# Kernel tuning notes

Hardware: AMD Instinct MI355X
Metric: run time of the kernel (lower is better)

Reference implementation:

```python
import jax, jax.numpy as jnp
import numpy as np

N = 50000   # nodes
E = 640000  # edges
G = 128     # graphs in batch
H = 128     # hidden_channels
F_NODE, F_EDGE, F_LIG, F_POC = 64, 16, 200, 100
N_STACK = 3  # num_layers - 1


def setup_inputs() -> dict:
    key = jax.random.key(0)
    ks = jax.random.split(key, 24)
    r = lambda i, shape, s=0.05: jax.random.normal(ks[i], shape, dtype=jnp.float32) * s
    z = lambda shape: jnp.zeros(shape, jnp.float32)
    return {
        "x": jax.random.normal(ks[0], (N, F_NODE), dtype=jnp.float32),
        "edge_index": jax.random.randint(ks[1], (2, E), 0, N),
        "edge_attr": jax.random.normal(ks[2], (E, F_EDGE), dtype=jnp.float32),
        "batch": jnp.sort(jax.random.randint(ks[3], (N,), 0, G)),
        "ligand_features": jax.random.normal(ks[4], (G, F_LIG), dtype=jnp.float32),
        "pocket_features": jax.random.normal(ks[5], (G, F_POC), dtype=jnp.float32),
        # conv1 (in != out -> lin_self is a Linear)
        "W1_msg": r(6, (F_NODE, H)), "b1_msg": z((H,)),
        "W1_edge": r(7, (F_EDGE, H)), "b1_edge": z((H,)),
        "W1_self": r(8, (F_NODE, H)), "b1_self": z((H,)),
        # stacked convs (in == out -> lin_self is Identity)
        "Wk_msg": r(9, (N_STACK, H, H)), "bk_msg": z((N_STACK, H)),
        "Wk_edge": r(10, (N_STACK, F_EDGE, H)), "bk_edge": z((N_STACK, H)),
        # global feature / fusion / output heads
        "Wl": r(11, (F_LIG, H)), "bl": z((H,)),
        "Wp": r(12, (F_POC, H)), "bp": z((H,)),
        "Wf": r(13, (3 * H, H)), "bf": z((H,)),
        "Wo": r(14, (H, 1)), "bo": z((1,)),
        "return_embeddings": 0,
    }


def _general_conv(x, edge_index, edge_attr, W_msg, b_msg, W_edge, b_edge, self_out):
    # PyG GeneralConv: msg = lin_msg(x_src) + lin_edge(edge_attr), sum-aggregated at dst,
    # then + lin_self(x) (Identity skip when passed self_out = x).
    src, dst = edge_index[0], edge_index[1]
    edge_term = edge_attr @ W_edge + b_edge            # [E, H] (per-edge, layer-specific)
    msg = x[src] @ W_msg + b_msg + edge_term           # [E, H] gather + GEMM
    agg = jax.ops.segment_sum(msg, dst, num_segments=x.shape[0])  # scatter-add
    return agg + self_out


def reference(x, edge_index, edge_attr, batch, ligand_features, pocket_features,
              W1_msg, b1_msg, W1_edge, b1_edge, W1_self, b1_self,
              Wk_msg, bk_msg, Wk_edge, bk_edge,
              Wl, bl, Wp, bp, Wf, bf, Wo, bo, return_embeddings):
    # conv1 with linear self-connection
    h = _general_conv(x, edge_index, edge_attr, W1_msg, b1_msg, W1_edge, b1_edge,
                      x @ W1_self + b1_self)
    h = jax.nn.relu(h)
    # stacked convs with identity self-connection
    for i in range(N_STACK):
        h = _general_conv(h, edge_index, edge_attr, Wk_msg[i], bk_msg[i],
                          Wk_edge[i], bk_edge[i], h)
        h = jax.nn.relu(h)
    # global mean pool over graphs
    sums = jax.ops.segment_sum(h, batch, num_segments=G)
    counts = jax.ops.segment_sum(jnp.ones((h.shape[0],), h.dtype), batch, num_segments=G)
    pooled = sums / jnp.maximum(counts, 1.0)[:, None]
    # global feature fusion
    lig = ligand_features @ Wl + bl
    poc = pocket_features @ Wp + bp
    fused = jnp.concatenate([pooled, lig, poc], axis=1) @ Wf + bf
    # dropout is a no-op in eval mode
    if not return_embeddings:
        fused = fused @ Wo + bo
    return fused
```

## Files before the change

kernel.cpp:

```cpp
#include <hip/hip_runtime.h>
#include <cstdint>

#define NN 50000
#define NE 640000
#define NG 128
#define HD 128
#define FN 64
#define FE 16
#define FL 200
#define FPOC 100
#define NSTACK 3

typedef unsigned short ushort_t;
typedef short short8 __attribute__((ext_vector_type(8)));
typedef float f32x4 __attribute__((ext_vector_type(4)));

__device__ __forceinline__ ushort_t f2bf(float f) {
    unsigned u = __float_as_uint(f);
    unsigned r = (u + 0x7fffu + ((u >> 16) & 1u)) >> 16;
    return (ushort_t)r;
}
__device__ __forceinline__ float bf2f(ushort_t u) {
    return __uint_as_float(((unsigned)u) << 16);
}


__global__ void count_kernel(const int* __restrict__ ei, int* __restrict__ cnt) {
    int e = blockIdx.x * 256 + threadIdx.x;
    if (e < NE) atomicAdd(&cnt[ei[NE + e]], 1);
}

__global__ void bsum_kernel(const int* __restrict__ cnt, int* __restrict__ bsum) {
    __shared__ int s[256];
    int t = threadIdx.x;
    int i = blockIdx.x * 256 + t;
    int v = (i < NN) ? cnt[i] : 0;
    s[t] = v;
    __syncthreads();
    for (int off = 128; off > 0; off >>= 1) {
        if (t < off) s[t] += s[t + off];
        __syncthreads();
    }
    if (t == 0) bsum[blockIdx.x] = s[0];
}

__global__ void bscan_kernel(const int* __restrict__ bsum, int* __restrict__ bpre, int nb) {
    __shared__ int s[256];
    int t = threadIdx.x;
    int v = (t < nb) ? bsum[t] : 0;
    s[t] = v;
    __syncthreads();
    for (int off = 1; off < 256; off <<= 1) {
        int w = (t >= off) ? s[t - off] : 0;
        __syncthreads();
        s[t] += w;
        __syncthreads();
    }
    if (t < nb) bpre[t] = s[t] - v;
}

__global__ void rowptr_kernel(const int* __restrict__ cnt, const int* __restrict__ bpre,
                              int* __restrict__ row_ptr) {
    __shared__ int s[256];
    int t = threadIdx.x;
    int i = blockIdx.x * 256 + t;
    int v = (i < NN) ? cnt[i] : 0;
    s[t] = v;
    __syncthreads();
    for (int off = 1; off < 256; off <<= 1) {
        int w = (t >= off) ? s[t - off] : 0;
        __syncthreads();
        s[t] += w;
        __syncthreads();
    }
    if (i < NN) row_ptr[i] = s[t] - v + bpre[blockIdx.x];
    if (i == 0) row_ptr[NN] = NE;
}

__global__ void fill_kernel(const int* __restrict__ ei, const int* __restrict__ row_ptr,
                            int* __restrict__ cnt, int2* __restrict__ csr) {
    int e = blockIdx.x * 256 + threadIdx.x;
    if (e < NE) {
        int s = ei[e];
        int d = ei[NE + e];
        int old = atomicSub(&cnt[d], 1);
        csr[row_ptr[d] + old - 1] = make_int2(s, e);
    }
}

__global__ __launch_bounds__(256) void sege_kernel(
    const int* __restrict__ row_ptr, const int2* __restrict__ csr,
    const float* __restrict__ ea, ushort_t* __restrict__ segaug) {
    int node = blockIdx.x * 4 + (threadIdx.x >> 6);
    if (node >= NN) return;
    int lane = threadIdx.x & 63;
    int G = lane >> 2, q4 = (lane & 3) * 4;
    int beg = row_ptr[node], end = row_ptr[node + 1];
    float4 a = make_float4(0.f, 0.f, 0.f, 0.f);
    for (int j = beg + G; j < end; j += 16) {
        int e = csr[j].y;
        float4 v = *(const float4*)(ea + (size_t)e * FE + q4);
        a.x += v.x; a.y += v.y; a.z += v.z; a.w += v.w;
    }
    for (int m = 4; m <= 32; m <<= 1) {
        a.x += __shfl_xor(a.x, m);
        a.y += __shfl_xor(a.y, m);
        a.z += __shfl_xor(a.z, m);
        a.w += __shfl_xor(a.w, m);
    }
    if (lane < 4) {
        ushort_t o[4] = {f2bf(a.x), f2bf(a.y), f2bf(a.z), f2bf(a.w)};
        *(uint2*)(segaug + (size_t)node * 32 + lane * 4) = *(uint2*)o;
    } else if (lane < 8) {
        ushort_t o[4] = {0, 0, 0, 0};
        if (lane == 4) { o[0] = f2bf((float)(end - beg)); o[1] = f2bf(1.f); }
        *(uint2*)(segaug + (size_t)node * 32 + lane * 4) = *(uint2*)o;
    }
}


__global__ void repack_kernel(const float* __restrict__ W1_msg,
                              const float* __restrict__ W1_self,
                              const float* __restrict__ W1_edge,
                              const float* __restrict__ b1_msg,
                              const float* __restrict__ b1_edge,
                              const float* __restrict__ b1_self,
                              const float* __restrict__ Wk_msg,
                              const float* __restrict__ Wk_edge,
                              const float* __restrict__ bk_msg,
                              const float* __restrict__ bk_edge,
                              ushort_t* __restrict__ pack) {
    int mid = blockIdx.y;
    const float *W = nullptr, *bm = nullptr, *be = nullptr, *bc = nullptr;
    int K;
    size_t doff;
    bool aug = false;
    if (mid == 0)      { W = W1_msg;  K = 64;  doff = 0; }
    else if (mid == 1) { W = W1_self; K = 64;  doff = 8192; }
    else if (mid == 2) { W = W1_edge; bm = b1_msg; be = b1_edge; bc = b1_self;
                         K = 32; doff = 16384; aug = true; }
    else if (mid <= 5) { int i = mid - 3; W = Wk_msg + (size_t)i * HD * HD;
                         K = 128; doff = 20480 + (size_t)i * 16384; }
    else               { int i = mid - 6; W = Wk_edge + (size_t)i * FE * HD;
                         bm = bk_msg + i * HD; be = bk_edge + i * HD;
                         K = 32; doff = 69632 + (size_t)i * 4096; aug = true; }
    int KS = K / 32;
    int t = blockIdx.x * 256 + threadIdx.x;
    if (t >= 8 * KS * 64) return;
    int lane = t & 63;
    int nk = t >> 6;
    int ks = nk % KS, nt = nk / KS;
    int n = nt * 16 + (lane & 15);
    int kb = ks * 32 + (lane >> 4) * 8;
    ushort_t o[8];
#pragma unroll
    for (int j = 0; j < 8; ++j) {
        int k = kb + j;
        float v;
        if (!aug)         v = W[(size_t)k * HD + n];
        else if (k < 16)  v = W[(size_t)k * HD + n];
        else if (k == 16) v = bm[n] + be[n];
        else if (k == 17) v = bc ? bc[n] : 0.f;
        else              v = 0.f;
        o[j] = f2bf(v);
    }
    *(uint4*)(pack + doff + (size_t)t * 8) = *(uint4*)o;
}


__global__ __launch_bounds__(256) void gemm_mfma_conv1(const float* __restrict__ A,
                                                       const ushort_t* __restrict__ segaug,
                                                       const ushort_t* __restrict__ pack,
                                                       ushort_t* __restrict__ Cm,
                                                       ushort_t* __restrict__ Cs, int n) {
    constexpr int STR = 72, SSTR = 40;
    __shared__ __align__(16) ushort_t As[64 * STR];
    __shared__ __align__(16) ushort_t Ss[64 * SSTR];
    int tid = threadIdx.x;
    int row0 = blockIdx.x * 64;
#pragma unroll
    for (int p = 0; p < 2; ++p) {
        int c = p * 256 + tid;
        int r = c >> 3, col = (c & 7) * 8;
        int gr = row0 + r;
        float4 f0 = make_float4(0.f, 0.f, 0.f, 0.f), f1 = f0;
        if (gr < n) {
            f0 = *(const float4*)(A + (size_t)gr * FN + col);
            f1 = *(const float4*)(A + (size_t)gr * FN + col + 4);
        }
        ushort_t o[8] = {f2bf(f0.x), f2bf(f0.y), f2bf(f0.z), f2bf(f0.w),
                         f2bf(f1.x), f2bf(f1.y), f2bf(f1.z), f2bf(f1.w)};
        *(uint4*)(&As[r * STR + col]) = *(uint4*)o;
    }
    {
        int c = tid;
        int r = c >> 2, col = (c & 3) * 8;
        int gr = row0 + r;
        uint4 v = make_uint4(0u, 0u, 0u, 0u);
        if (gr < n) v = *(const uint4*)(segaug + (size_t)gr * 32 + col);
        *(uint4*)(&Ss[r * SSTR + col]) = v;
    }
    __syncthreads();
    int lane = tid & 63, wave = tid >> 6;
    int m = lane & 15, quad = lane >> 4;
    f32x4 acc[16];
#pragma unroll
    for (int i = 0; i < 16; ++i) acc[i] = (f32x4)(0.f);
    const short8* Bmsg = (const short8*)pack;
    const short8* Bself = (const short8*)(pack + 8192);
    const short8* Beaug = (const short8*)(pack + 16384);
#pragma unroll
    for (int ks = 0; ks < 2; ++ks) {
        short8 a = *(const short8*)(&As[(wave * 16 + m) * STR + ks * 32 + quad * 8]);
#pragma unroll
        for (int nt = 0; nt < 8; ++nt) {
            acc[nt] = __builtin_amdgcn_mfma_f32_16x16x32_bf16(
                a, Bmsg[(nt * 2 + ks) * 64 + lane], acc[nt], 0, 0, 0);
            acc[8 + nt] = __builtin_amdgcn_mfma_f32_16x16x32_bf16(
                a, Bself[(nt * 2 + ks) * 64 + lane], acc[8 + nt], 0, 0, 0);
        }
    }
    {
        short8 sa = *(const short8*)(&Ss[(wave * 16 + m) * SSTR + quad * 8]);
#pragma unroll
        for (int nt = 0; nt < 8; ++nt)
            acc[8 + nt] = __builtin_amdgcn_mfma_f32_16x16x32_bf16(
                sa, Beaug[nt * 64 + lane], acc[8 + nt], 0, 0, 0);
    }
#pragma unroll
    for (int nt = 0; nt < 8; ++nt) {
        int col = nt * 16 + m;
#pragma unroll
        for (int r = 0; r < 4; ++r) {
            int grow = row0 + wave * 16 + quad * 4 + r;
            if (grow < n) {
                Cm[(size_t)grow * HD + col] = f2bf(acc[nt][r]);
                Cs[(size_t)grow * HD + col] = f2bf(acc[8 + nt][r]);
            }
        }
    }
}


__device__ __forceinline__ void accum8(float* a, uint4 v) {
    a[0] += __uint_as_float(v.x << 16);
    a[1] += __uint_as_float(v.x & 0xffff0000u);
    a[2] += __uint_as_float(v.y << 16);
    a[3] += __uint_as_float(v.y & 0xffff0000u);
    a[4] += __uint_as_float(v.z << 16);
    a[5] += __uint_as_float(v.z & 0xffff0000u);
    a[6] += __uint_as_float(v.w << 16);
    a[7] += __uint_as_float(v.w & 0xffff0000u);
}

__global__ __launch_bounds__(256, 6) void fused_agg_gemm(
    const int* __restrict__ row_ptr, const int2* __restrict__ csr,
    const ushort_t* __restrict__ msg_in, const ushort_t* __restrict__ S_in,
    const ushort_t* __restrict__ segaug, const ushort_t* __restrict__ Bm,
    const ushort_t* __restrict__ Be, ushort_t* __restrict__ msg_out,
    ushort_t* __restrict__ S_out) {
    constexpr int STR = 136, SSTR = 40;
    __shared__ __align__(16) ushort_t Hs[16 * STR];
    __shared__ __align__(16) ushort_t Ss[16 * SSTR];
    int tid = threadIdx.x;
    int node0 = blockIdx.x * 16;
    if (tid < 64) {
        int r = tid >> 2, col = (tid & 3) * 8;
        *(uint4*)(&Ss[r * SSTR + col]) =
            *(const uint4*)(segaug + (size_t)(node0 + r) * 32 + col);
    }
    int nl = tid >> 4;
    int node = node0 + nl;
    int c8 = (tid & 15) * 8;
    int beg = row_ptr[node], end = row_ptr[node + 1];
    float a0[8] = {0.f, 0.f, 0.f, 0.f, 0.f, 0.f, 0.f, 0.f};
    float a1[8] = {0.f, 0.f, 0.f, 0.f, 0.f, 0.f, 0.f, 0.f};
    int j = beg;
    for (; j + 3 < end; j += 4) {
        int u0 = csr[j].x, u1 = csr[j + 1].x, u2 = csr[j + 2].x, u3 = csr[j + 3].x;
        uint4 v0 = *(const uint4*)(msg_in + (size_t)u0 * HD + c8);
        uint4 v1 = *(const uint4*)(msg_in + (size_t)u1 * HD + c8);
        uint4 v2 = *(const uint4*)(msg_in + (size_t)u2 * HD + c8);
        uint4 v3 = *(const uint4*)(msg_in + (size_t)u3 * HD + c8);
        accum8(a0, v0);
        accum8(a1, v1);
        accum8(a0, v2);
        accum8(a1, v3);
    }
    for (; j < end; ++j) {
        uint4 v = *(const uint4*)(msg_in + (size_t)csr[j].x * HD + c8);
        accum8(a0, v);
    }
    accum8(a0, *(const uint4*)(S_in + (size_t)node * HD + c8));
    {
        ushort_t h8[8];
#pragma unroll
        for (int i = 0; i < 8; ++i) h8[i] = f2bf(fmaxf(a0[i] + a1[i], 0.f));
        *(uint4*)(&Hs[nl * STR + c8]) = *(uint4*)h8;
    }
    __syncthreads();
    int lane = tid & 63, wave = tid >> 6;
    int m = lane & 15, quad = lane >> 4;
    f32x4 acc[2], accE[2];
#pragma unroll
    for (int t = 0; t < 2; ++t) { acc[t] = (f32x4)(0.f); accE[t] = (f32x4)(0.f); }
    const short8* Bmv = (const short8*)Bm;
    const short8* Bev = (const short8*)Be;
#pragma unroll
    for (int ks = 0; ks < 4; ++ks) {
        short8 a = *(const short8*)(&Hs[m * STR + ks * 32 + quad * 8]);
#pragma unroll
        for (int t = 0; t < 2; ++t) {
            int nt = wave * 2 + t;
            acc[t] = __builtin_amdgcn_mfma_f32_16x16x32_bf16(
                a, Bmv[(nt * 4 + ks) * 64 + lane], acc[t], 0, 0, 0);
        }
    }
    {
        short8 sa = *(const short8*)(&Ss[m * SSTR + quad * 8]);
#pragma unroll
        for (int t = 0; t < 2; ++t) {
            int nt = wave * 2 + t;
            accE[t] = __builtin_amdgcn_mfma_f32_16x16x32_bf16(
                sa, Bev[nt * 64 + lane], accE[t], 0, 0, 0);
        }
    }
#pragma unroll
    for (int t = 0; t < 2; ++t) {
        int col = (wave * 2 + t) * 16 + m;
#pragma unroll
        for (int r = 0; r < 4; ++r) {
            int rl = quad * 4 + r;
            size_t gidx = (size_t)(node0 + rl) * HD + col;
            msg_out[gidx] = f2bf(acc[t][r]);
            S_out[gidx] = f2bf(accE[t][r] + bf2f(Hs[rl * STR + col]));
        }
    }
}


__global__ __launch_bounds__(256, 6) void agg_kernel(
    const int* __restrict__ row_ptr, const int2* __restrict__ csr,
    const ushort_t* __restrict__ xm, const ushort_t* __restrict__ selfb,
    ushort_t* __restrict__ out, int n) {
    int tid = threadIdx.x;
    int node = blockIdx.x * 16 + (tid >> 4);
    if (node >= n) return;
    int c8 = (tid & 15) * 8;
    int beg = row_ptr[node], end = row_ptr[node + 1];
    float a0[8] = {0.f, 0.f, 0.f, 0.f, 0.f, 0.f, 0.f, 0.f};
    float a1[8] = {0.f, 0.f, 0.f, 0.f, 0.f, 0.f, 0.f, 0.f};
    int j = beg;
    for (; j + 3 < end; j += 4) {
        int u0 = csr[j].x, u1 = csr[j + 1].x, u2 = csr[j + 2].x, u3 = csr[j + 3].x;
        uint4 v0 = *(const uint4*)(xm + (size_t)u0 * HD + c8);
        uint4 v1 = *(const uint4*)(xm + (size_t)u1 * HD + c8);
        uint4 v2 = *(const uint4*)(xm + (size_t)u2 * HD + c8);
        uint4 v3 = *(const uint4*)(xm + (size_t)u3 * HD + c8);
        accum8(a0, v0);
        accum8(a1, v1);
        accum8(a0, v2);
        accum8(a1, v3);
    }
    for (; j < end; ++j) {
        uint4 v = *(const uint4*)(xm + (size_t)csr[j].x * HD + c8);
        accum8(a0, v);
    }
    accum8(a0, *(const uint4*)(selfb + (size_t)node * HD + c8));
    ushort_t o[8];
#pragma unroll
    for (int i = 0; i < 8; ++i) o[i] = f2bf(fmaxf(a0[i] + a1[i], 0.f));
    *(uint4*)(out + (size_t)node * HD + c8) = *(uint4*)o;
}


__global__ void pool_partial(const ushort_t* __restrict__ h, const int* __restrict__ batch,
                             float* __restrict__ pooled4) {
    int g = blockIdx.x;
    int q = blockIdx.y;
    int f = threadIdx.x;
    int lo = 0, hi = NN;
    while (lo < hi) { int m = (lo + hi) >> 1; if (batch[m] < g) lo = m + 1; else hi = m; }
    int s = lo;
    lo = s; hi = NN;
    while (lo < hi) { int m = (lo + hi) >> 1; if (batch[m] < g + 1) lo = m + 1; else hi = m; }
    int e = lo;
    int len = e - s;
    int c0 = s + (len * q) / 4;
    int c1 = s + (len * (q + 1)) / 4;
    float acc = 0.f;
    for (int v = c0; v < c1; ++v) acc += bf2f(h[(size_t)v * HD + f]);
    pooled4[((size_t)q * NG + g) * HD + f] = acc;
}


__global__ void head_kernel(const float* __restrict__ pooled4, const int* __restrict__ batch,
                            const float* __restrict__ lf, const float* __restrict__ pfe,
                            const float* __restrict__ Wl, const float* __restrict__ bl,
                            const float* __restrict__ Wp, const float* __restrict__ bp,
                            const float* __restrict__ Wf, const float* __restrict__ bfv,
                            const float* __restrict__ Wo, const float* __restrict__ bo,
                            float* __restrict__ out) {
    __shared__ float cat[3 * HD];
    __shared__ float red[HD];
    int g = blockIdx.x, j = threadIdx.x;
    int lo = 0, hi = NN;
    while (lo < hi) { int m = (lo + hi) >> 1; if (batch[m] < g) lo = m + 1; else hi = m; }
    int s0 = lo;
    lo = s0; hi = NN;
    while (lo < hi) { int m = (lo + hi) >> 1; if (batch[m] < g + 1) lo = m + 1; else hi = m; }
    float cntf = (float)(lo - s0);
    float p = pooled4[(size_t)g * HD + j] + pooled4[((size_t)NG + g) * HD + j] +
              pooled4[((size_t)2 * NG + g) * HD + j] + pooled4[((size_t)3 * NG + g) * HD + j];
    cat[j] = p / fmaxf(cntf, 1.f);
    float s = bl[j];
    for (int k = 0; k < FL; ++k) s += lf[g * FL + k] * Wl[k * HD + j];
    cat[HD + j] = s;
    s = bp[j];
    for (int k = 0; k < FPOC; ++k) s += pfe[g * FPOC + k] * Wp[k * HD + j];
    cat[2 * HD + j] = s;
    __syncthreads();
    float fj = bfv[j];
    for (int k = 0; k < 3 * HD; ++k) fj += cat[k] * Wf[k * HD + j];
    red[j] = fj * Wo[j];
    __syncthreads();
    for (int off = 64; off > 0; off >>= 1) {
        if (j < off) red[j] += red[j + off];
        __syncthreads();
    }
    if (j == 0) out[g] = red[0] + bo[0];
}


extern "C" void kernel_launch(void* const* d_in, const int* in_sizes, int n_in,
                              void* d_out, int out_size, void* d_ws, size_t ws_size,
                              hipStream_t stream) {
    const float* x       = (const float*)d_in[0];
    const int*   ei      = (const int*)d_in[1];
    const float* ea      = (const float*)d_in[2];
    const int*   batch   = (const int*)d_in[3];
    const float* lf      = (const float*)d_in[4];
    const float* pfe     = (const float*)d_in[5];
    const float* W1_msg  = (const float*)d_in[6];
    const float* b1_msg  = (const float*)d_in[7];
    const float* W1_edge = (const float*)d_in[8];
    const float* b1_edge = (const float*)d_in[9];
    const float* W1_self = (const float*)d_in[10];
    const float* b1_self = (const float*)d_in[11];
    const float* Wk_msg  = (const float*)d_in[12];
    const float* bk_msg  = (const float*)d_in[13];
    const float* Wk_edge = (const float*)d_in[14];
    const float* bk_edge = (const float*)d_in[15];
    const float* Wl      = (const float*)d_in[16];
    const float* bl      = (const float*)d_in[17];
    const float* Wp      = (const float*)d_in[18];
    const float* bp      = (const float*)d_in[19];
    const float* Wf      = (const float*)d_in[20];
    const float* bfv     = (const float*)d_in[21];
    const float* Wo      = (const float*)d_in[22];
    const float* bo      = (const float*)d_in[23];

    char* wsp = (char*)d_ws;
    size_t off = 0;
    auto carve = [&](size_t bytes) -> void* {
        char* p = wsp + off;
        off += (bytes + 255) & ~(size_t)255;
        return (void*)p;
    };
    int*      cnt     = (int*)carve((size_t)NN * 4);
    int*      row_ptr = (int*)carve((size_t)(NN + 1) * 4);
    int2*     csr     = (int2*)carve((size_t)NE * 8);
    ushort_t* segaug  = (ushort_t*)carve((size_t)NN * 32 * 2);
    ushort_t* pack    = (ushort_t*)carve((size_t)81920 * 2);
    ushort_t* bufC    = (ushort_t*)carve((size_t)NN * HD * 2);
    ushort_t* bufD    = (ushort_t*)carve((size_t)NN * HD * 2);
    ushort_t* bufS    = (ushort_t*)carve((size_t)NN * HD * 2);
    ushort_t* bufT    = (ushort_t*)carve((size_t)NN * HD * 2);
    float*    pooled4 = (float*)carve((size_t)4 * NG * HD * 4);
    int*      bsum    = (int*)carve((size_t)256 * 4);
    int*      bpre    = (int*)carve((size_t)256 * 4);

    const int NBLK = (NN + 255) / 256;

    hipMemsetAsync(cnt, 0, (size_t)NN * 4, stream);

    count_kernel<<<(NE + 255) / 256, 256, 0, stream>>>(ei, cnt);
    bsum_kernel<<<NBLK, 256, 0, stream>>>(cnt, bsum);
    bscan_kernel<<<1, 256, 0, stream>>>(bsum, bpre, NBLK);
    rowptr_kernel<<<NBLK, 256, 0, stream>>>(cnt, bpre, row_ptr);
    fill_kernel<<<(NE + 255) / 256, 256, 0, stream>>>(ei, row_ptr, cnt, csr);
    sege_kernel<<<(NN + 3) / 4, 256, 0, stream>>>(row_ptr, csr, ea, segaug);
    repack_kernel<<<dim3(8, 9), 256, 0, stream>>>(W1_msg, W1_self, W1_edge, b1_msg,
                                                  b1_edge, b1_self, Wk_msg, Wk_edge,
                                                  bk_msg, bk_edge, pack);

    gemm_mfma_conv1<<<dim3((NN + 63) / 64), 256, 0, stream>>>(x, segaug, pack, bufC,
                                                              bufS, NN);
    fused_agg_gemm<<<NN / 16, 256, 0, stream>>>(row_ptr, csr, bufC, bufS, segaug,
                                                pack + 20480, pack + 69632, bufD, bufT);
    fused_agg_gemm<<<NN / 16, 256, 0, stream>>>(row_ptr, csr, bufD, bufT, segaug,
                                                pack + 20480 + 16384, pack + 69632 + 4096,
                                                bufC, bufS);
    fused_agg_gemm<<<NN / 16, 256, 0, stream>>>(row_ptr, csr, bufC, bufS, segaug,
                                                pack + 20480 + 32768, pack + 69632 + 8192,
                                                bufD, bufT);
    agg_kernel<<<(NN + 15) / 16, 256, 0, stream>>>(row_ptr, csr, bufD, bufT, bufC, NN);

    pool_partial<<<dim3(NG, 4), HD, 0, stream>>>(bufC, batch, pooled4);
    head_kernel<<<NG, HD, 0, stream>>>(pooled4, batch, lf, pfe, Wl, bl, Wp, bp, Wf, bfv,
                                       Wo, bo, (float*)d_out);
}
```

Baseline: 414.1 us.

## Bucket edges by destination block before CSR fill to localize scatter

```diff
diff --git a/kernel.cpp b/kernel.cpp
--- a/kernel.cpp
+++ b/kernel.cpp
@@ -10,6 +10,8 @@
 #define FL 200
 #define FPOC 100
 #define NSTACK 3
+#define NBUCK 782
+#define BCAP 1536
 
 typedef unsigned short ushort_t;
 typedef short short8 __attribute__((ext_vector_type(8)));
@@ -25,9 +27,17 @@
 }
 
 
-__global__ void count_kernel(const int* __restrict__ ei, int* __restrict__ cnt) {
+__global__ void countbucket_kernel(const int* __restrict__ ei, int* __restrict__ cnt,
+                                   int* __restrict__ bcnt, int2* __restrict__ bents) {
     int e = blockIdx.x * 256 + threadIdx.x;
-    if (e < NE) atomicAdd(&cnt[ei[NE + e]], 1);
+    if (e < NE) {
+        int s = ei[e];
+        int d = ei[NE + e];
+        atomicAdd(&cnt[d], 1);
+        int b = d >> 6;
+        int off = atomicAdd(&bcnt[b], 1);
+        bents[(size_t)b * BCAP + off] = make_int2(s, (e << 6) | (d & 63));
+    }
 }
 
 __global__ void bsum_kernel(const int* __restrict__ cnt, int* __restrict__ bsum) {
@@ -77,14 +87,17 @@
     if (i == 0) row_ptr[NN] = NE;
 }
 
-__global__ void fill_kernel(const int* __restrict__ ei, const int* __restrict__ row_ptr,
-                            int* __restrict__ cnt, int2* __restrict__ csr) {
-    int e = blockIdx.x * 256 + threadIdx.x;
-    if (e < NE) {
-        int s = ei[e];
-        int d = ei[NE + e];
+__global__ void place_kernel(const int* __restrict__ bcnt, const int2* __restrict__ bents,
+                             const int* __restrict__ row_ptr, int* __restrict__ cnt,
+                             int2* __restrict__ csr) {
+    int b = blockIdx.x;
+    int n = bcnt[b];
+    for (int i = threadIdx.x; i < n; i += 256) {
+        int2 en = bents[(size_t)b * BCAP + i];
+        int d = (b << 6) | (en.y & 63);
+        int eid = en.y >> 6;
         int old = atomicSub(&cnt[d], 1);
-        csr[row_ptr[d] + old - 1] = make_int2(s, e);
+        csr[row_ptr[d] + old - 1] = make_int2(en.x, eid);
     }
 }
 
@@ -467,7 +480,8 @@
         off += (bytes + 255) & ~(size_t)255;
         return (void*)p;
     };
-    int*      cnt     = (int*)carve((size_t)NN * 4);
+    int*      cnt     = (int*)carve((size_t)(NN + NBUCK) * 4);
+    int*      bcnt    = cnt + NN;
     int*      row_ptr = (int*)carve((size_t)(NN + 1) * 4);
     int2*     csr     = (int2*)carve((size_t)NE * 8);
     ushort_t* segaug  = (ushort_t*)carve((size_t)NN * 32 * 2);
@@ -479,16 +493,17 @@
     float*    pooled4 = (float*)carve((size_t)4 * NG * HD * 4);
     int*      bsum    = (int*)carve((size_t)256 * 4);
     int*      bpre    = (int*)carve((size_t)256 * 4);
+    int2*     bents   = (int2*)bufC;
 
     const int NBLK = (NN + 255) / 256;
 
-    hipMemsetAsync(cnt, 0, (size_t)NN * 4, stream);
-
-    count_kernel<<<(NE + 255) / 256, 256, 0, stream>>>(ei, cnt);
+    hipMemsetAsync(cnt, 0, (size_t)(NN + NBUCK) * 4, stream);
+
+    countbucket_kernel<<<(NE + 255) / 256, 256, 0, stream>>>(ei, cnt, bcnt, bents);
     bsum_kernel<<<NBLK, 256, 0, stream>>>(cnt, bsum);
     bscan_kernel<<<1, 256, 0, stream>>>(bsum, bpre, NBLK);
     rowptr_kernel<<<NBLK, 256, 0, stream>>>(cnt, bpre, row_ptr);
-    fill_kernel<<<(NE + 255) / 256, 256, 0, stream>>>(ei, row_ptr, cnt, csr);
+    place_kernel<<<NBUCK, 256, 0, stream>>>(bcnt, bents, row_ptr, cnt, csr);
     sege_kernel<<<(NN + 3) / 4, 256, 0, stream>>>(row_ptr, csr, ea, segaug);
     repack_kernel<<<dim3(8, 9), 256, 0, stream>>>(W1_msg, W1_self, W1_edge, b1_msg,
                                                   b1_edge, b1_self, Wk_msg, Wk_edge,
```

Result: slower. 556.5 us (+34.4%).
